# Kernel optimization log

Hardware: AMD Instinct MI355X
Metric: run time of the kernel (lower is better)

Reference implementation:

```python
import jax, jax.numpy as jnp
import numpy as np

IM_SIZE = (128, 128)  # N_i per image dim
N_BATCH, N_COILS, N_TRJ = 1, 8, 8192


def _image_grid(im_size):
    # r_i in [-1/2, 1/2): (arange(N_i) - N_i//2) / N_i, flattened to (R, d)
    axes = [(jnp.arange(n, dtype=jnp.float32) - n // 2) / n for n in im_size]
    mesh = jnp.meshgrid(*axes, indexing='ij')
    return jnp.stack([m.reshape(-1) for m in mesh], axis=-1)  # (R, d)


def setup_inputs() -> dict:
    key = jax.random.key(0)
    k1, k2, k3 = jax.random.split(key, 3)
    img_real = jax.random.normal(k1, (N_BATCH, N_COILS) + IM_SIZE, dtype=jnp.float32)
    img_imag = jax.random.normal(k2, (N_BATCH, N_COILS) + IM_SIZE, dtype=jnp.float32)
    # trajectory k_i uniform in [-N_i/2, N_i/2]
    scale = jnp.asarray(IM_SIZE, dtype=jnp.float32)
    trj = (jax.random.uniform(k3, (N_BATCH, N_TRJ, len(IM_SIZE)), dtype=jnp.float32) - 0.5) * scale
    return {"img_real": img_real, "img_imag": img_imag, "trj": trj}


def reference(img_real, img_imag, trj):
    # matrix_nufft.forward: ksp[n,c,k] = sum_r img[n,c,r] * exp(-j 2 pi k . r)
    d = trj.shape[-1]
    im_size = img_real.shape[-d:]
    grid = _image_grid(im_size)                              # (R, d)
    phase = jnp.einsum('nkd,rd->nkr', trj, grid)             # (N, K, R)
    A = jnp.exp(-2j * jnp.pi * phase)                        # (N, K, R) complex64
    img = (img_real + 1j * img_imag).reshape(img_real.shape[0], -1, grid.shape[0])  # (N, C, R)
    ksp = jnp.einsum('nkr,ncr->nck', A, img)                 # (N, C, K) complex64
    # return real/imag stacked on last axis (harness-friendly real output)
    return jnp.stack([ksp.real, ksp.imag], axis=-1)          # (N, C, K, 2)
```

## Files before the change

kernel.cpp:

```cpp
#include <hip/hip_runtime.h>
#include <math.h>


#define K_TOTAL 8192
#define KB      128
#define NX      128
#define NY      128

typedef short  bf16x8 __attribute__((ext_vector_type(8)));
typedef float  f32x4  __attribute__((ext_vector_type(4)));

__device__ inline unsigned short f32_to_bf16_rne(float f) {
    unsigned int u = __float_as_uint(f);
    u += 0x7FFFu + ((u >> 16) & 1u);
    return (unsigned short)(u >> 16);
}
__device__ inline unsigned pack2(float a, float b) {
    return (unsigned)f32_to_bf16_rne(a) | ((unsigned)f32_to_bf16_rne(b) << 16);
}

__global__ __launch_bounds__(512, 2) void nufft_mfma_kernel(
    const float* __restrict__ imgR,
    const float* __restrict__ imgI,
    const float* __restrict__ trj,
    float* __restrict__ out)
{
    __shared__ __align__(16) unsigned short slab[2][128 * 128];

    const int tid = threadIdx.x;
    const int bid = blockIdx.x;
    const int c   = bid >> 6;
    const int kg0 = (bid & 63) * KB;

    const int wave = tid >> 6;
    const int lane = tid & 63;
    const int l15  = lane & 15;
    const int lg   = lane >> 4;

    const int rowgrp = tid >> 5;
    const int seg    = tid & 31;

    {
        float4 R0, I0, R1, I1;
        const float* bR = imgR + (c * NX) * NY + seg * 4;
        const float* bI = imgI + (c * NX) * NY + seg * 4;

        R0 = *(const float4*)(bR + rowgrp * NY);
        I0 = *(const float4*)(bI + rowgrp * NY);
#pragma unroll
        for (int i = 0; i < 8; ++i) {
            const bool even = (i & 1) == 0;
            if (i < 7) {
                const int rown = rowgrp + 16 * (i + 1);
                if (even) { R1 = *(const float4*)(bR + rown * NY);
                            I1 = *(const float4*)(bI + rown * NY); }
                else      { R0 = *(const float4*)(bR + rown * NY);
                            I0 = *(const float4*)(bI + rown * NY); }
            }
            const float4 vR = even ? R0 : R1;
            const float4 vI = even ? I0 : I1;
            const int row = rowgrp + 16 * i;
            const int off = row * 256 + ((seg * 8) ^ ((row & 15) << 4));
            uint2 v;
            v.x = pack2(vR.x, vR.y); v.y = pack2(vR.z, vR.w);
            *(uint2*)((char*)&slab[0][0] + off) = v;
            v.x = pack2(vI.x, vI.y); v.y = pack2(vI.z, vI.w);
            *(uint2*)((char*)&slab[1][0] + off) = v;
        }
    }

    bf16x8 aR[4], aI[4];
    {
        const float ky = trj[(kg0 + wave * 16 + l15) * 2 + 1];
        float u = -ky * (1.0f / 128.0f); u -= floorf(u);
        float s1i, s1r; __sincosf(6.283185307179586f * u, &s1i, &s1r);
#pragma unroll
        for (int ys = 0; ys < 4; ++ys) {
            const int y0 = ys * 32 + lg * 8;
            float t = -ky * (float)(y0 - 64) * (1.0f / 128.0f); t -= floorf(t);
            float ci_, cr_; __sincosf(6.283185307179586f * t, &ci_, &cr_);
#pragma unroll
            for (int m = 0; m < 8; ++m) {
                aR[ys][m] = (short)f32_to_bf16_rne(cr_);
                aI[ys][m] = (short)f32_to_bf16_rne(ci_);
                const float nr = cr_ * s1r - ci_ * s1i;
                ci_ = cr_ * s1i + ci_ * s1r;
                cr_ = nr;
            }
        }
    }

    float kxv[4];
#pragma unroll
    for (int j = 0; j < 4; ++j)
        kxv[j] = trj[(kg0 + wave * 16 + lg * 4 + j) * 2 + 0];

    __syncthreads();

    const char* sbR = (const char*)&slab[0][0];
    const char* sbI = (const char*)&slab[1][0];

    f32x4 outRe = {0,0,0,0};
    f32x4 outIm = {0,0,0,0};

#pragma unroll
    for (int nt = 0; nt < 8; ++nt) {
        const int x    = nt * 16 + l15;
        const int rowb = x * 256;

        f32x4 P = {0,0,0,0}, Q = {0,0,0,0}, U = {0,0,0,0}, V = {0,0,0,0};
#pragma unroll
        for (int ys = 0; ys < 4; ++ys) {
            const int inb = (lg * 16 + ys * 64) ^ (l15 << 4);
            const bf16x8 bR = *(const bf16x8*)(sbR + rowb + inb);
            const bf16x8 bI = *(const bf16x8*)(sbI + rowb + inb);
            P = __builtin_amdgcn_mfma_f32_16x16x32_bf16(aR[ys], bR, P, 0, 0, 0);
            Q = __builtin_amdgcn_mfma_f32_16x16x32_bf16(aI[ys], bI, Q, 0, 0, 0);
            U = __builtin_amdgcn_mfma_f32_16x16x32_bf16(aR[ys], bI, U, 0, 0, 0);
            V = __builtin_amdgcn_mfma_f32_16x16x32_bf16(aI[ys], bR, V, 0, 0, 0);
        }

        const float rx = (float)(x - 64) * (1.0f / 128.0f);
#pragma unroll
        for (int j = 0; j < 4; ++j) {
            float t = -kxv[j] * rx; t -= floorf(t);
            float eI_, eR_; __sincosf(6.283185307179586f * t, &eI_, &eR_);
            const float TR = P[j] - Q[j];
            const float TI = U[j] + V[j];
            outRe[j] += eR_ * TR - eI_ * TI;
            outIm[j] += eR_ * TI + eI_ * TR;
        }
    }

#pragma unroll
    for (int j = 0; j < 4; ++j) {
        float r_ = outRe[j];
        float i_ = outIm[j];
#pragma unroll
        for (int m = 1; m < 16; m <<= 1) {
            r_ += __shfl_xor(r_, m, 64);
            i_ += __shfl_xor(i_, m, 64);
        }
        if (l15 == 0) {
            const int kg = kg0 + wave * 16 + lg * 4 + j;
            ((float2*)out)[c * K_TOTAL + kg] = make_float2(r_, i_);
        }
    }
}

extern "C" void kernel_launch(void* const* d_in, const int* in_sizes, int n_in,
                              void* d_out, int out_size, void* d_ws, size_t ws_size,
                              hipStream_t stream) {
    const float* imgR = (const float*)d_in[0];
    const float* imgI = (const float*)d_in[1];
    const float* trj  = (const float*)d_in[2];
    float* out = (float*)d_out;

    hipLaunchKernelGGL(nufft_mfma_kernel, dim3(512), dim3(512), 0, stream,
                       imgR, imgI, trj, out);
}
```

Before: 20.89 us.

## Pre-convert image to swizzled bf16 in workspace and stream via global_load_lds

Adds a small pre-pass kernel that converts each coil's float image to bf16 once per call and writes it in the swizzled LDS layout to the workspace. The main kernel then copies its slab straight into LDS with global_load_lds 16-byte transfers, instead of every block loading fp32, converting and storing to LDS. This removes redundant conversion work (64 blocks per coil each redid it) and halves global read volume in exchange for an extra kernel launch and a workspace round trip. Synchronization still relies on the existing __syncthreads before the LDS reads.

```diff
diff --git a/kernel.cpp b/kernel.cpp
--- a/kernel.cpp
+++ b/kernel.cpp
@@ -9,6 +9,7 @@
 
 typedef short  bf16x8 __attribute__((ext_vector_type(8)));
 typedef float  f32x4  __attribute__((ext_vector_type(4)));
+typedef unsigned int u32;
 
 __device__ inline unsigned short f32_to_bf16_rne(float f) {
     unsigned int u = __float_as_uint(f);
@@ -18,14 +19,36 @@
 __device__ inline unsigned pack2(float a, float b) {
     return (unsigned)f32_to_bf16_rne(a) | ((unsigned)f32_to_bf16_rne(b) << 16);
 }
+__device__ inline void gload_lds16(const void* g, void* l) {
+    __builtin_amdgcn_global_load_lds(
+        (const __attribute__((address_space(1))) u32*)g,
+        (__attribute__((address_space(3))) u32*)l, 16, 0, 0);
+}
+
+__global__ void cvt_swz_kernel(const float* __restrict__ imgR,
+                               const float* __restrict__ imgI,
+                               unsigned short* __restrict__ ws) {
+    const int tid   = blockIdx.x * 256 + threadIdx.x;
+    const int col4  = tid & 31;
+    const int row   = (tid >> 5) & 127;
+    const int plane = (tid >> 12) & 1;
+    const int c     = tid >> 13;
+    const float* src = plane ? imgI : imgR;
+    const float4 v = *(const float4*)(src + (c * NX + row) * NY + col4 * 4);
+    uint2 p;
+    p.x = pack2(v.x, v.y);
+    p.y = pack2(v.z, v.w);
+    char* dst = (char*)ws + c * 65536 + plane * 32768 + row * 256
+              + ((col4 * 8) ^ ((row & 15) << 4));
+    *(uint2*)dst = p;
+}
 
 __global__ __launch_bounds__(512, 2) void nufft_mfma_kernel(
-    const float* __restrict__ imgR,
-    const float* __restrict__ imgI,
+    const unsigned short* __restrict__ ws,
     const float* __restrict__ trj,
     float* __restrict__ out)
 {
-    __shared__ __align__(16) unsigned short slab[2][128 * 128];
+    __shared__ __align__(1024) unsigned short slab[2][128 * 128];
 
     const int tid = threadIdx.x;
     const int bid = blockIdx.x;
@@ -37,36 +60,13 @@
     const int l15  = lane & 15;
     const int lg   = lane >> 4;
 
-    const int rowgrp = tid >> 5;
-    const int seg    = tid & 31;
-
     {
-        float4 R0, I0, R1, I1;
-        const float* bR = imgR + (c * NX) * NY + seg * 4;
-        const float* bI = imgI + (c * NX) * NY + seg * 4;
-
-        R0 = *(const float4*)(bR + rowgrp * NY);
-        I0 = *(const float4*)(bI + rowgrp * NY);
+        const char* gbase = (const char*)ws + (size_t)c * 65536
+                          + (size_t)wave * 8192 + (size_t)lane * 16;
+        char* lbase = (char*)&slab[0][0] + wave * 8192;
 #pragma unroll
-        for (int i = 0; i < 8; ++i) {
-            const bool even = (i & 1) == 0;
-            if (i < 7) {
-                const int rown = rowgrp + 16 * (i + 1);
-                if (even) { R1 = *(const float4*)(bR + rown * NY);
-                            I1 = *(const float4*)(bI + rown * NY); }
-                else      { R0 = *(const float4*)(bR + rown * NY);
-                            I0 = *(const float4*)(bI + rown * NY); }
-            }
-            const float4 vR = even ? R0 : R1;
-            const float4 vI = even ? I0 : I1;
-            const int row = rowgrp + 16 * i;
-            const int off = row * 256 + ((seg * 8) ^ ((row & 15) << 4));
-            uint2 v;
-            v.x = pack2(vR.x, vR.y); v.y = pack2(vR.z, vR.w);
-            *(uint2*)((char*)&slab[0][0] + off) = v;
-            v.x = pack2(vI.x, vI.y); v.y = pack2(vI.z, vI.w);
-            *(uint2*)((char*)&slab[1][0] + off) = v;
-        }
+        for (int j = 0; j < 8; ++j)
+            gload_lds16(gbase + j * 1024, lbase + j * 1024);
     }
 
     bf16x8 aR[4], aI[4];
@@ -155,7 +155,10 @@
     const float* imgI = (const float*)d_in[1];
     const float* trj  = (const float*)d_in[2];
     float* out = (float*)d_out;
+    unsigned short* ws = (unsigned short*)d_ws;
 
+    hipLaunchKernelGGL(cvt_swz_kernel, dim3(256), dim3(256), 0, stream,
+                       imgR, imgI, ws);
     hipLaunchKernelGGL(nufft_mfma_kernel, dim3(512), dim3(512), 0, stream,
-                       imgR, imgI, trj, out);
+                       ws, trj, out);
 }
```

Result: slower. 25.47 us (+21.9%).
